# Kernel tuning notes

Measured on AMD Instinct MI355X. Metric: run time of the kernel, lower is better.

Reference implementation:

```python
import jax, jax.numpy as jnp
import numpy as np
import math

H = 16  # heads
EPS_NORM = 1e-12
EPS_W = 1e-6


def setup_inputs() -> dict:
    key = jax.random.key(0)
    ks = jax.random.split(key, 6)
    B, T, d = 2, 2048, 1024
    s = 1.0 / math.sqrt(d)
    return {
        "x": jax.random.normal(ks[0], (B, T, d), dtype=jnp.float32),
        "Wq": jax.random.normal(ks[1], (d, d), dtype=jnp.float32) * s,
        "Wk": jax.random.normal(ks[2], (d, d), dtype=jnp.float32) * s,
        "Wv": jax.random.normal(ks[3], (d, d), dtype=jnp.float32) * s,
        "Wo": jax.random.normal(ks[4], (d, d), dtype=jnp.float32) * s,
        "bo": jnp.zeros((d,), dtype=jnp.float32),
    }


def _l2norm(t):
    # F.normalize(dim=-1): x / max(||x||, eps)
    n = jnp.sqrt(jnp.sum(t * t, axis=-1, keepdims=True))
    return t / jnp.maximum(n, EPS_NORM)


def reference(x, Wq, Wk, Wv, Wo, bo):
    B, T, d = x.shape
    dk = d // H
    # projections (torch Linear: y = x @ W.T), split heads -> [B, H, T, dk]
    def proj(W):
        return (x @ W.T).reshape(B, T, H, dk).transpose(0, 2, 1, 3)
    Q = _l2norm(proj(Wq))
    K = _l2norm(proj(Wk))
    V = proj(Wv)
    # angular similarity scores [B, H, T, T]
    sim = jnp.clip(jnp.einsum("bhqd,bhkd->bhqk", Q, K), -0.999, 0.999)
    scores = 1.0 - jnp.arccos(sim) / jnp.float32(math.pi)
    W = jnp.maximum(scores, EPS_W) ** 8
    W = W / (jnp.sum(W, axis=-1, keepdims=True) + EPS_W)
    out = jnp.einsum("bhqk,bhkd->bhqd", W, V)  # [B, H, T, dk]
    out = out.transpose(0, 2, 1, 3).reshape(B, T, d)
    return out @ Wo.T + bo
```

## Files before the change

### kernel.cpp

```cpp
#include <hip/hip_runtime.h>
#include <hip/hip_bf16.h>
#include <hip/hip_fp16.h>
#include <math.h>

#define BB 2
#define TT 2048
#define DD 1024
#define HH 16
#define DK 64
#define KT 64

typedef _Float16 f16x8 __attribute__((ext_vector_type(8)));
typedef __fp16 fp16x2 __attribute__((ext_vector_type(2)));
typedef __attribute__((ext_vector_type(4))) float f32x4;
typedef __attribute__((ext_vector_type(2))) float f32x2;

static __device__ __forceinline__ void g2lds16(const void* g, void* l) {
    __builtin_amdgcn_global_load_lds(
        (const __attribute__((address_space(1))) unsigned int*)g,
        (__attribute__((address_space(3))) unsigned int*)l, 16, 0, 0);
}

static __device__ __forceinline__ f32x2 w8pair(f32x2 s, f32x2& rs) {
    f32x2 ax;
    ax.x = fminf(fabsf(s.x), 0.999f);
    ax.y = fminf(fabsf(s.y), 0.999f);
    f32x2 p = ax * -0.0059617f + 0.0236380f;
    p = p * ax + (-0.0675180f);
    p = p * ax + 0.49997851f;
    f32x2 om = 1.0f - ax;
    f32x2 u;
    u.x = sqrtf(om.x);
    u.y = sqrtf(om.y);
    f32x2 uq = u * p;
    f32x2 e = 0.5f - uq;
    f32x2 t;
    t.x = 0.5f + copysignf(e.x, s.x);
    t.y = 0.5f + copysignf(e.y, s.y);
    f32x2 t2 = t * t;
    f32x2 t4 = t2 * t2;
    f32x2 t8 = t4 * t4;
    rs += t8;
    return t8;
}
static __device__ __forceinline__ int packh2(f32x2 v) {
    union { fp16x2 h; int i; } u;
    u.h = __builtin_amdgcn_cvt_pkrtz(v.x, v.y);
    return u.i;
}

__global__ __launch_bounds__(256) void cvtall_kernel(
    const float* __restrict__ x,  const float* __restrict__ Wq,
    const float* __restrict__ Wk, const float* __restrict__ Wv,
    const float* __restrict__ Wo,
    _Float16* __restrict__ xh, _Float16* __restrict__ W3h,
    _Float16* __restrict__ Woh)
{
    const int bid = blockIdx.x;
    const float* s; _Float16* d; int blk;
    if (bid < 2048) { s = x; d = xh; blk = bid; }
    else {
        const int idx = bid - 2048;
        const int w   = idx >> 9;
        blk = idx & 511;
        s = (w == 0) ? Wq : (w == 1) ? Wk : (w == 2) ? Wv : Wo;
        d = (w == 3) ? Woh : W3h + (size_t)w * (DD * DD);
    }
    const int i = (blk * 256 + threadIdx.x) * 8;
    float4 a = *(const float4*)(s + i);
    float4 b = *(const float4*)(s + i + 4);
    union { _Float16 h[8]; int4 v; } u;
    u.h[0] = (_Float16)a.x; u.h[1] = (_Float16)a.y;
    u.h[2] = (_Float16)a.z; u.h[3] = (_Float16)a.w;
    u.h[4] = (_Float16)b.x; u.h[5] = (_Float16)b.y;
    u.h[6] = (_Float16)b.z; u.h[7] = (_Float16)b.w;
    *(int4*)(d + i) = u.v;
}

template<int NPROD, int EPI>
__global__ __launch_bounds__(256, NPROD == 1 ? 3 : 2) void gemm_f16_128(
    const _Float16* __restrict__ Ah_g, const _Float16* __restrict__ Al_g,
    const _Float16* __restrict__ B_g, const float* __restrict__ bias,
    float* __restrict__ C,
    _Float16* __restrict__ Qh, _Float16* __restrict__ Kh,
    _Float16* __restrict__ Vh,
    int nbx, int K, int hasBias)
{
    __shared__ _Float16 Ahs[8][128][8];
    __shared__ _Float16 Bhs[8][128][8];
    __shared__ _Float16 Als[NPROD == 2 ? 8 : 1][128][8];

    const int nwg  = gridDim.x;
    const int wgid = blockIdx.x;
    const int cpx  = nwg >> 3;
    const int swz  = (wgid & 7) * cpx + (wgid >> 3);
    const int by   = swz / nbx;
    const int bx   = swz - by * nbx;

    const int t    = threadIdx.x;
    const int m0   = by * 128;
    const int n0g  = bx * 128;
    const int seg  = n0g >> 10;
    const int n0   = n0g & 1023;

    const int lane = t & 63;
    const int w    = t >> 6;
    const int wm   = w >> 1;
    const int wn   = w & 1;
    const int l15  = lane & 15;
    const int quad = lane >> 4;

    f32x4 acc[4][4];
#pragma unroll
    for (int i = 0; i < 4; ++i)
#pragma unroll
        for (int j = 0; j < 4; ++j) acc[i][j] = (f32x4)0.f;

    for (int k0 = 0; k0 < K; k0 += 64) {
        __syncthreads();
#pragma unroll
        for (int i = 0; i < 2; ++i) {
            const int cc = w * 2 + i;
#pragma unroll
            for (int half = 0; half < 2; ++half) {
                g2lds16(Ah_g + (size_t)(m0 + half * 64 + lane) * K + k0 + cc * 8,
                        &Ahs[cc][half * 64][0]);
                if (NPROD == 2)
                    g2lds16(Al_g + (size_t)(m0 + half * 64 + lane) * K + k0 + cc * 8,
                            &Als[cc][half * 64][0]);
                g2lds16(B_g + (size_t)(n0g + half * 64 + lane) * K + k0 + cc * 8,
                        &Bhs[cc][half * 64][0]);
            }
        }
        __syncthreads();

#pragma unroll
        for (int kh = 0; kh < 2; ++kh) {
            f16x8 ah[4], bh[4];
#pragma unroll
            for (int tm = 0; tm < 4; ++tm)
                ah[tm] = *(const f16x8*)&Ahs[kh * 4 + quad][wm * 64 + tm * 16 + l15][0];
#pragma unroll
            for (int tn = 0; tn < 4; ++tn)
                bh[tn] = *(const f16x8*)&Bhs[kh * 4 + quad][wn * 64 + tn * 16 + l15][0];
#pragma unroll
            for (int tm = 0; tm < 4; ++tm)
#pragma unroll
                for (int tn = 0; tn < 4; ++tn)
                    acc[tm][tn] = __builtin_amdgcn_mfma_f32_16x16x32_f16(
                        ah[tm], bh[tn], acc[tm][tn], 0, 0, 0);
            if (NPROD == 2) {
                f16x8 al[4];
#pragma unroll
                for (int tm = 0; tm < 4; ++tm)
                    al[tm] = *(const f16x8*)&Als[kh * 4 + quad][wm * 64 + tm * 16 + l15][0];
#pragma unroll
                for (int tm = 0; tm < 4; ++tm)
#pragma unroll
                    for (int tn = 0; tn < 4; ++tn)
                        acc[tm][tn] = __builtin_amdgcn_mfma_f32_16x16x32_f16(
                            al[tm], bh[tn], acc[tm][tn], 0, 0, 0);
            }
        }
    }

    if (EPI == 0) {
#pragma unroll
        for (int tm = 0; tm < 4; ++tm)
#pragma unroll
            for (int tn = 0; tn < 4; ++tn) {
                const int col  = n0 + wn * 64 + tn * 16 + l15;
                const float bv = hasBias ? bias[col] : 0.f;
                const int rowb = m0 + wm * 64 + tm * 16 + quad * 4;
#pragma unroll
                for (int r = 0; r < 4; ++r)
                    C[(size_t)(rowb + r) * 1024 + col] = acc[tm][tn][r] + bv;
            }
    } else {
        if (seg < 2) {
            _Float16* __restrict__ dstb = (seg == 0) ? Qh : Kh;
            const int hh = (n0 >> 6) + wn;
#pragma unroll
            for (int tm = 0; tm < 4; ++tm) {
#pragma unroll
                for (int r = 0; r < 4; ++r) {
                    float ss = 0.f;
#pragma unroll
                    for (int tn = 0; tn < 4; ++tn) {
                        const float v = acc[tm][tn][r];
                        ss += v * v;
                    }
                    ss += __shfl_xor(ss, 1);
                    ss += __shfl_xor(ss, 2);
                    ss += __shfl_xor(ss, 4);
                    ss += __shfl_xor(ss, 8);
                    const float inv = rsqrtf(fmaxf(ss, 1e-24f));
                    const int row = m0 + wm * 64 + tm * 16 + quad * 4 + r;
                    const int b   = row >> 11;
                    const int tt  = row & 2047;
                    _Float16* dst = dstb + ((size_t)(b * HH + hh) * TT + tt) * DK;
#pragma unroll
                    for (int tn = 0; tn < 4; ++tn)
                        dst[tn * 16 + l15] = (_Float16)(acc[tm][tn][r] * inv);
                }
            }
        } else {
#pragma unroll
            for (int tm = 0; tm < 4; ++tm)
#pragma unroll
                for (int tn = 0; tn < 4; ++tn) {
                    const int col  = n0 + wn * 64 + tn * 16 + l15;
                    const int rowb = m0 + wm * 64 + tm * 16 + quad * 4;
#pragma unroll
                    for (int r = 0; r < 4; ++r)
                        Vh[(size_t)(rowb + r) * 1024 + col] =
                            (_Float16)acc[tm][tn][r];
                }
        }
    }
}

__global__ __launch_bounds__(256) void vtrans_kernel(
    const _Float16* __restrict__ Vh, _Float16* __restrict__ Vt)
{
    __shared__ _Float16 Vtmp[64][72];
    const int t  = threadIdx.x;
    const int t0 = blockIdx.x * 64;
    const int h  = blockIdx.y;
    const int b  = blockIdx.z;

    {
        const int i  = t >> 2;
        const int jc = (t & 3) * 16;
        const _Float16* src = Vh + (size_t)(b * TT + t0 + i) * DD + h * DK + jc;
        f16x8 a = *(const f16x8*)(src);
        f16x8 c = *(const f16x8*)(src + 8);
#pragma unroll
        for (int e = 0; e < 8; ++e) {
            Vtmp[jc + e][i]     = a[e];
            Vtmp[jc + 8 + e][i] = c[e];
        }
    }
    __syncthreads();
    {
        const int d  = t >> 2;
        const int kc = (t & 3) * 16;
        _Float16* dst = Vt + ((size_t)((b * HH + h) * DK + d)) * TT + t0 + kc;
        *(int4*)(dst)     = *(const int4*)&Vtmp[d][kc];
        *(int4*)(dst + 8) = *(const int4*)&Vtmp[d][kc + 8];
    }
}

__global__ __launch_bounds__(256, 4) void attn_kernel(
    const _Float16* __restrict__ Qh_g, const _Float16* __restrict__ Kh_g,
    const _Float16* __restrict__ Vt_g,
    _Float16* __restrict__ Oh, _Float16* __restrict__ Ol)
{
    __shared__ _Float16 Vts[2][8][64][8];
    __shared__ _Float16 Ws[2][64][72];
    __shared__ float Rbuf[4][64];
    __shared__ float Rfin[64];

    const int t    = threadIdx.x;
    const int lane = t & 63;
    const int w    = t >> 6;
    const int l15  = lane & 15;
    const int quad = lane >> 4;
    const int q0   = blockIdx.x * 64;
    const int h    = blockIdx.y;
    const int b    = blockIdx.z;
    const size_t bh = (size_t)(b * HH + h);

    const _Float16* kh_g = Kh_g + bh * TT * DK;
    const _Float16* vt_g = Vt_g + bh * (size_t)DK * TT;

    f16x8 qf[4][2];
#pragma unroll
    for (int qt = 0; qt < 4; ++qt)
#pragma unroll
        for (int s = 0; s < 2; ++s)
            qf[qt][s] = *(const f16x8*)(Qh_g + (bh * TT + q0 + qt * 16 + l15) * DK
                                        + s * 32 + quad * 8);

    f16x8 kf[2], kfn[2];
#pragma unroll
    for (int s = 0; s < 2; ++s) {
        kf[s] = *(const f16x8*)(kh_g
            + (size_t)(w * 16 + l15) * DK + s * 32 + quad * 8);
        kfn[s] = kf[s];
    }

#pragma unroll
    for (int j = 0; j < 2; ++j) {
        const int kc = w * 2 + j;
        g2lds16(vt_g + (size_t)lane * TT + kc * 8, &Vts[0][kc][0][0]);
    }

    f32x4 acc[4];
#pragma unroll
    for (int j = 0; j < 4; ++j) acc[j] = (f32x4)0.f;
    f32x2 rs2[4];
#pragma unroll
    for (int j = 0; j < 4; ++j) rs2[j] = (f32x2)0.f;

    int p = 0;
    for (int k0 = 0; k0 < TT; k0 += KT, p ^= 1) {
        const int kn = k0 + KT;
        if (kn < TT) {
#pragma unroll
            for (int s = 0; s < 2; ++s)
                kfn[s] = *(const f16x8*)(kh_g
                    + (size_t)(kn + w * 16 + l15) * DK + s * 32 + quad * 8);
        }

#pragma unroll
        for (int qt = 0; qt < 4; ++qt) {
            f32x4 c_ = (f32x4)0.f;
#pragma unroll
            for (int s = 0; s < 2; ++s)
                c_ = __builtin_amdgcn_mfma_f32_16x16x32_f16(
                    kf[s], qf[qt][s], c_, 0, 0, 0);
            f32x2 p01, p23;
            p01.x = c_[0]; p01.y = c_[1];
            p23.x = c_[2]; p23.y = c_[3];
            f32x2 w01 = w8pair(p01, rs2[qt]);
            f32x2 w23 = w8pair(p23, rs2[qt]);
            int2 pk;
            pk.x = packh2(w01);
            pk.y = packh2(w23);
            *(int2*)&Ws[p][qt * 16 + l15][w * 16 + quad * 4] = pk;
        }
        __syncthreads();

        if (kn < TT) {
#pragma unroll
            for (int j = 0; j < 2; ++j) {
                const int kc = w * 2 + j;
                g2lds16(vt_g + (size_t)lane * TT + kn + kc * 8,
                        &Vts[p ^ 1][kc][0][0]);
            }
        }

#pragma unroll
        for (int kstep = 0; kstep < 2; ++kstep) {
            f16x8 av = *(const f16x8*)&Ws[p][16 * w + l15][kstep * 32 + quad * 8];
#pragma unroll
            for (int nd = 0; nd < 4; ++nd) {
                f16x8 bv = *(const f16x8*)&Vts[p][kstep * 4 + quad][nd * 16 + l15][0];
                acc[nd] = __builtin_amdgcn_mfma_f32_16x16x32_f16(
                    av, bv, acc[nd], 0, 0, 0);
            }
        }

#pragma unroll
        for (int s = 0; s < 2; ++s)
            kf[s] = kfn[s];
    }

#pragma unroll
    for (int qt = 0; qt < 4; ++qt) {
        float pr = rs2[qt].x + rs2[qt].y;
        pr += __shfl_xor(pr, 16);
        pr += __shfl_xor(pr, 32);
        if (quad == 0) Rbuf[w][qt * 16 + l15] = pr;
    }
    __syncthreads();
    if (t < 64) {
        float s = Rbuf[0][t] + Rbuf[1][t] + Rbuf[2][t] + Rbuf[3][t];
        Rfin[t] = 1.f / (s + 1e-6f);
    }
    __syncthreads();

#pragma unroll
    for (int r = 0; r < 4; ++r) {
        const int q = 16 * w + quad * 4 + r;
        const float inv = Rfin[q];
        const size_t base = (size_t)(b * TT + q0 + q) * DD + h * DK + l15;
#pragma unroll
        for (int nd = 0; nd < 4; ++nd) {
            float v = acc[nd][r] * inv;
            _Float16 hv = (_Float16)v;
            Oh[base + nd * 16] = hv;
            Ol[base + nd * 16] = (_Float16)(v - (float)hv);
        }
    }
}

extern "C" void kernel_launch(void* const* d_in, const int* in_sizes, int n_in,
                              void* d_out, int out_size, void* d_ws, size_t ws_size,
                              hipStream_t stream)
{
    const float* x  = (const float*)d_in[0];
    const float* Wq = (const float*)d_in[1];
    const float* Wk = (const float*)d_in[2];
    const float* Wv = (const float*)d_in[3];
    const float* Wo = (const float*)d_in[4];
    const float* bo = (const float*)d_in[5];
    float* out = (float*)d_out;

    const int M = BB * TT;
    const int K = DD;

    const size_t MB = 1024 * 1024;
    char* ws = (char*)d_ws;
    _Float16* xh  = (_Float16*)(ws);
    _Float16* W3h = (_Float16*)(ws + 8 * MB);
    _Float16* Woh = (_Float16*)(ws + 14 * MB);
    _Float16* Qh  = (_Float16*)(ws + 16 * MB);
    _Float16* Kh  = (_Float16*)(ws + 24 * MB);
    _Float16* Vh  = (_Float16*)(ws + 32 * MB);
    _Float16* Vt  = (_Float16*)(ws + 40 * MB);
    _Float16* Oh  = (_Float16*)(ws);
    _Float16* Ol  = (_Float16*)(ws + 32 * MB);

    dim3 gB(256);

    cvtall_kernel<<<4096, gB, 0, stream>>>(x, Wq, Wk, Wv, Wo, xh, W3h, Woh);

    {
        const int nbx = 3072 / 128;
        const int nby = M / 128;
        gemm_f16_128<1, 1><<<nbx * nby, gB, 0, stream>>>(
            xh, nullptr, W3h, nullptr, nullptr, Qh, Kh, Vh, nbx, K, 0);
    }

    vtrans_kernel<<<dim3(TT / 64, HH, BB), gB, 0, stream>>>(Vh, Vt);

    attn_kernel<<<dim3(TT / 64, HH, BB), gB, 0, stream>>>(Qh, Kh, Vt, Oh, Ol);

    {
        const int nbx = 1024 / 128;
        const int nby = M / 128;
        gemm_f16_128<2, 0><<<nbx * nby, gB, 0, stream>>>(
            Oh, Ol, Woh, bo, out, nullptr, nullptr, nullptr, nbx, K, 1);
    }
}
```

Before: 310.8 us.

## Split GEMM template, double-buffer output GEMM, retile V layout, use raw sqrt/rsq

Splits the templated GEMM into a QKV-projection kernel and a separate output-projection kernel. The output kernel double-buffers its LDS tiles so the next K-slice loads overlap the current MFMAs. The transposed V buffer is stored in 8-column chunk blocks so the attention kernel's global-to-LDS loads read contiguous 1 KB runs instead of strided rows. The sqrt in the angular weight and the rsqrt in normalization are replaced with hardware builtins to drop IEEE correction code. The doubled LDS in the output GEMM may lower its occupancy.

```diff
diff --git a/kernel.cpp b/kernel.cpp
--- a/kernel.cpp
+++ b/kernel.cpp
@@ -30,8 +30,8 @@
     p = p * ax + 0.49997851f;
     f32x2 om = 1.0f - ax;
     f32x2 u;
-    u.x = sqrtf(om.x);
-    u.y = sqrtf(om.y);
+    u.x = __builtin_amdgcn_sqrtf(om.x);
+    u.y = __builtin_amdgcn_sqrtf(om.y);
     f32x2 uq = u * p;
     f32x2 e = 0.5f - uq;
     f32x2 t;
@@ -77,18 +77,13 @@
     *(int4*)(d + i) = u.v;
 }
 
-template<int NPROD, int EPI>
-__global__ __launch_bounds__(256, NPROD == 1 ? 3 : 2) void gemm_f16_128(
-    const _Float16* __restrict__ Ah_g, const _Float16* __restrict__ Al_g,
-    const _Float16* __restrict__ B_g, const float* __restrict__ bias,
-    float* __restrict__ C,
+__global__ __launch_bounds__(256, 3) void gemm_qkv(
+    const _Float16* __restrict__ Ah_g, const _Float16* __restrict__ B_g,
     _Float16* __restrict__ Qh, _Float16* __restrict__ Kh,
-    _Float16* __restrict__ Vh,
-    int nbx, int K, int hasBias)
+    _Float16* __restrict__ Vh, int nbx, int K)
 {
     __shared__ _Float16 Ahs[8][128][8];
     __shared__ _Float16 Bhs[8][128][8];
-    __shared__ _Float16 Als[NPROD == 2 ? 8 : 1][128][8];
 
     const int nwg  = gridDim.x;
     const int wgid = blockIdx.x;
@@ -125,9 +120,6 @@
             for (int half = 0; half < 2; ++half) {
                 g2lds16(Ah_g + (size_t)(m0 + half * 64 + lane) * K + k0 + cc * 8,
                         &Ahs[cc][half * 64][0]);
-                if (NPROD == 2)
-                    g2lds16(Al_g + (size_t)(m0 + half * 64 + lane) * K + k0 + cc * 8,
-                            &Als[cc][half * 64][0]);
                 g2lds16(B_g + (size_t)(n0g + half * 64 + lane) * K + k0 + cc * 8,
                         &Bhs[cc][half * 64][0]);
             }
@@ -149,75 +141,144 @@
                 for (int tn = 0; tn < 4; ++tn)
                     acc[tm][tn] = __builtin_amdgcn_mfma_f32_16x16x32_f16(
                         ah[tm], bh[tn], acc[tm][tn], 0, 0, 0);
-            if (NPROD == 2) {
-                f16x8 al[4];
-#pragma unroll
-                for (int tm = 0; tm < 4; ++tm)
-                    al[tm] = *(const f16x8*)&Als[kh * 4 + quad][wm * 64 + tm * 16 + l15][0];
-#pragma unroll
-                for (int tm = 0; tm < 4; ++tm)
-#pragma unroll
-                    for (int tn = 0; tn < 4; ++tn)
-                        acc[tm][tn] = __builtin_amdgcn_mfma_f32_16x16x32_f16(
-                            al[tm], bh[tn], acc[tm][tn], 0, 0, 0);
-            }
-        }
-    }
-
-    if (EPI == 0) {
+        }
+    }
+
+    if (seg < 2) {
+        _Float16* __restrict__ dstb = (seg == 0) ? Qh : Kh;
+        const int hh = (n0 >> 6) + wn;
+#pragma unroll
+        for (int tm = 0; tm < 4; ++tm) {
+#pragma unroll
+            for (int r = 0; r < 4; ++r) {
+                float ss = 0.f;
+#pragma unroll
+                for (int tn = 0; tn < 4; ++tn) {
+                    const float v = acc[tm][tn][r];
+                    ss += v * v;
+                }
+                ss += __shfl_xor(ss, 1);
+                ss += __shfl_xor(ss, 2);
+                ss += __shfl_xor(ss, 4);
+                ss += __shfl_xor(ss, 8);
+                const float inv = __builtin_amdgcn_rsqf(fmaxf(ss, 1e-24f));
+                const int row = m0 + wm * 64 + tm * 16 + quad * 4 + r;
+                const int b   = row >> 11;
+                const int tt  = row & 2047;
+                _Float16* dst = dstb + ((size_t)(b * HH + hh) * TT + tt) * DK;
+#pragma unroll
+                for (int tn = 0; tn < 4; ++tn)
+                    dst[tn * 16 + l15] = (_Float16)(acc[tm][tn][r] * inv);
+            }
+        }
+    } else {
 #pragma unroll
         for (int tm = 0; tm < 4; ++tm)
 #pragma unroll
             for (int tn = 0; tn < 4; ++tn) {
                 const int col  = n0 + wn * 64 + tn * 16 + l15;
-                const float bv = hasBias ? bias[col] : 0.f;
                 const int rowb = m0 + wm * 64 + tm * 16 + quad * 4;
 #pragma unroll
                 for (int r = 0; r < 4; ++r)
-                    C[(size_t)(rowb + r) * 1024 + col] = acc[tm][tn][r] + bv;
-            }
-    } else {
-        if (seg < 2) {
-            _Float16* __restrict__ dstb = (seg == 0) ? Qh : Kh;
-            const int hh = (n0 >> 6) + wn;
+                    Vh[(size_t)(rowb + r) * 1024 + col] =
+                        (_Float16)acc[tm][tn][r];
+            }
+    }
+}
+
+__global__ __launch_bounds__(256) void gemm_wo(
+    const _Float16* __restrict__ Ah_g, const _Float16* __restrict__ Al_g,
+    const _Float16* __restrict__ B_g, const float* __restrict__ bias,
+    float* __restrict__ C, int nbx, int K)
+{
+    __shared__ _Float16 Ahs[2][8][128][8];
+    __shared__ _Float16 Als[2][8][128][8];
+    __shared__ _Float16 Bhs[2][8][128][8];
+
+    const int nwg  = gridDim.x;
+    const int wgid = blockIdx.x;
+    const int cpx  = nwg >> 3;
+    const int swz  = (wgid & 7) * cpx + (wgid >> 3);
+    const int by   = swz / nbx;
+    const int bx   = swz - by * nbx;
+
+    const int t    = threadIdx.x;
+    const int m0   = by * 128;
+    const int n0g  = bx * 128;
+
+    const int lane = t & 63;
+    const int w    = t >> 6;
+    const int wm   = w >> 1;
+    const int wn   = w & 1;
+    const int l15  = lane & 15;
+    const int quad = lane >> 4;
+
+    f32x4 acc[4][4];
+#pragma unroll
+    for (int i = 0; i < 4; ++i)
+#pragma unroll
+        for (int j = 0; j < 4; ++j) acc[i][j] = (f32x4)0.f;
+
+    auto STAGE = [&](int bf, int k0) {
+#pragma unroll
+        for (int i = 0; i < 2; ++i) {
+            const int cc = w * 2 + i;
+#pragma unroll
+            for (int half = 0; half < 2; ++half) {
+                g2lds16(Ah_g + (size_t)(m0 + half * 64 + lane) * K + k0 + cc * 8,
+                        &Ahs[bf][cc][half * 64][0]);
+                g2lds16(Al_g + (size_t)(m0 + half * 64 + lane) * K + k0 + cc * 8,
+                        &Als[bf][cc][half * 64][0]);
+                g2lds16(B_g + (size_t)(n0g + half * 64 + lane) * K + k0 + cc * 8,
+                        &Bhs[bf][cc][half * 64][0]);
+            }
+        }
+    };
+
+    STAGE(0, 0);
+    int cur = 0;
+    for (int k0 = 0; k0 < K; k0 += 64) {
+        __syncthreads();
+        if (k0 + 64 < K) STAGE(cur ^ 1, k0 + 64);
+
+#pragma unroll
+        for (int kh = 0; kh < 2; ++kh) {
+            f16x8 ah[4], al[4], bh[4];
 #pragma unroll
             for (int tm = 0; tm < 4; ++tm) {
-#pragma unroll
-                for (int r = 0; r < 4; ++r) {
-                    float ss = 0.f;
-#pragma unroll
-                    for (int tn = 0; tn < 4; ++tn) {
-                        const float v = acc[tm][tn][r];
-                        ss += v * v;
-                    }
-                    ss += __shfl_xor(ss, 1);
-                    ss += __shfl_xor(ss, 2);
-                    ss += __shfl_xor(ss, 4);
-                    ss += __shfl_xor(ss, 8);
-                    const float inv = rsqrtf(fmaxf(ss, 1e-24f));
-                    const int row = m0 + wm * 64 + tm * 16 + quad * 4 + r;
-                    const int b   = row >> 11;
-                    const int tt  = row & 2047;
-                    _Float16* dst = dstb + ((size_t)(b * HH + hh) * TT + tt) * DK;
-#pragma unroll
-                    for (int tn = 0; tn < 4; ++tn)
-                        dst[tn * 16 + l15] = (_Float16)(acc[tm][tn][r] * inv);
-                }
-            }
-        } else {
+                ah[tm] = *(const f16x8*)&Ahs[cur][kh * 4 + quad][wm * 64 + tm * 16 + l15][0];
+                al[tm] = *(const f16x8*)&Als[cur][kh * 4 + quad][wm * 64 + tm * 16 + l15][0];
+            }
+#pragma unroll
+            for (int tn = 0; tn < 4; ++tn)
+                bh[tn] = *(const f16x8*)&Bhs[cur][kh * 4 + quad][wn * 64 + tn * 16 + l15][0];
 #pragma unroll
             for (int tm = 0; tm < 4; ++tm)
 #pragma unroll
-                for (int tn = 0; tn < 4; ++tn) {
-                    const int col  = n0 + wn * 64 + tn * 16 + l15;
-                    const int rowb = m0 + wm * 64 + tm * 16 + quad * 4;
-#pragma unroll
-                    for (int r = 0; r < 4; ++r)
-                        Vh[(size_t)(rowb + r) * 1024 + col] =
-                            (_Float16)acc[tm][tn][r];
-                }
-        }
-    }
+                for (int tn = 0; tn < 4; ++tn)
+                    acc[tm][tn] = __builtin_amdgcn_mfma_f32_16x16x32_f16(
+                        ah[tm], bh[tn], acc[tm][tn], 0, 0, 0);
+#pragma unroll
+            for (int tm = 0; tm < 4; ++tm)
+#pragma unroll
+                for (int tn = 0; tn < 4; ++tn)
+                    acc[tm][tn] = __builtin_amdgcn_mfma_f32_16x16x32_f16(
+                        al[tm], bh[tn], acc[tm][tn], 0, 0, 0);
+        }
+        cur ^= 1;
+    }
+
+#pragma unroll
+    for (int tm = 0; tm < 4; ++tm)
+#pragma unroll
+        for (int tn = 0; tn < 4; ++tn) {
+            const int col  = n0g + wn * 64 + tn * 16 + l15;
+            const float bv = bias[col];
+            const int rowb = m0 + wm * 64 + tm * 16 + quad * 4;
+#pragma unroll
+            for (int r = 0; r < 4; ++r)
+                C[(size_t)(rowb + r) * 1024 + col] = acc[tm][tn][r] + bv;
+        }
 }
 
 __global__ __launch_bounds__(256) void vtrans_kernel(
@@ -228,6 +289,7 @@
     const int t0 = blockIdx.x * 64;
     const int h  = blockIdx.y;
     const int b  = blockIdx.z;
+    const int bh = b * HH + h;
 
     {
         const int i  = t >> 2;
@@ -245,9 +307,10 @@
     {
         const int d  = t >> 2;
         const int kc = (t & 3) * 16;
-        _Float16* dst = Vt + ((size_t)((b * HH + h) * DK + d)) * TT + t0 + kc;
-        *(int4*)(dst)     = *(const int4*)&Vtmp[d][kc];
-        *(int4*)(dst + 8) = *(const int4*)&Vtmp[d][kc + 8];
+        const int tc = (t0 + kc) >> 3;
+        _Float16* dst = Vt + ((size_t)bh * (TT >> 3) + tc) * (64 * 8) + d * 8;
+        *(int4*)(dst)          = *(const int4*)&Vtmp[d][kc];
+        *(int4*)(dst + 64 * 8) = *(const int4*)&Vtmp[d][kc + 8];
     }
 }
 
@@ -272,7 +335,7 @@
     const size_t bh = (size_t)(b * HH + h);
 
     const _Float16* kh_g = Kh_g + bh * TT * DK;
-    const _Float16* vt_g = Vt_g + bh * (size_t)DK * TT;
+    const _Float16* vt_g = Vt_g + bh * (size_t)(TT >> 3) * (64 * 8);
 
     f16x8 qf[4][2];
 #pragma unroll
@@ -293,7 +356,7 @@
 #pragma unroll
     for (int j = 0; j < 2; ++j) {
         const int kc = w * 2 + j;
-        g2lds16(vt_g + (size_t)lane * TT + kc * 8, &Vts[0][kc][0][0]);
+        g2lds16(vt_g + (size_t)kc * (64 * 8) + lane * 8, &Vts[0][kc][0][0]);
     }
 
     f32x4 acc[4];
@@ -336,7 +399,7 @@
 #pragma unroll
             for (int j = 0; j < 2; ++j) {
                 const int kc = w * 2 + j;
-                g2lds16(vt_g + (size_t)lane * TT + kn + kc * 8,
+                g2lds16(vt_g + ((size_t)(kn >> 3) + kc) * (64 * 8) + lane * 8,
                         &Vts[p ^ 1][kc][0][0]);
             }
         }
@@ -399,7 +462,6 @@
     float* out = (float*)d_out;
 
     const int M = BB * TT;
-    const int K = DD;
 
     const size_t MB = 1024 * 1024;
     char* ws = (char*)d_ws;
@@ -420,8 +482,8 @@
     {
         const int nbx = 3072 / 128;
         const int nby = M / 128;
-        gemm_f16_128<1, 1><<<nbx * nby, gB, 0, stream>>>(
-            xh, nullptr, W3h, nullptr, nullptr, Qh, Kh, Vh, nbx, K, 0);
+        gemm_qkv<<<nbx * nby, gB, 0, stream>>>(
+            xh, W3h, Qh, Kh, Vh, nbx, DD);
     }
 
     vtrans_kernel<<<dim3(TT / 64, HH, BB), gB, 0, stream>>>(Vh, Vt);
@@ -431,7 +493,7 @@
     {
         const int nbx = 1024 / 128;
         const int nby = M / 128;
-        gemm_f16_128<2, 0><<<nbx * nby, gB, 0, stream>>>(
-            Oh, Ol, Woh, bo, out, nullptr, nullptr, nullptr, nbx, K, 1);
-    }
-}
+        gemm_wo<<<nbx * nby, gB, 0, stream>>>(
+            Oh, Ol, Woh, bo, out, nbx, DD);
+    }
+}
```

Result: faster. 262.9 us (-15.4%).
